# Kernel tuning notes

Measured on AMD Instinct MI355X. Metric: run time of the kernel, lower is better.

The kernel has to match this reference:

```python
import jax, jax.numpy as jnp
import numpy as np


def setup_inputs() -> dict:
    key = jax.random.key(0)
    k1, k2 = jax.random.split(key)
    B, D = 8192, 256
    pred = jax.random.normal(k1, (B, D), dtype=jnp.float32)
    gt = jax.random.normal(k2, (B, D), dtype=jnp.float32)
    sigma = jnp.ones((), dtype=jnp.float32)  # learned scalar param (dim=1, mode='auto')
    return {"pred": pred, "gt": gt, "sigma": sigma}


def reference(pred, gt, sigma):
    # p, g: [B, D] (flatten from start_dim=1 is identity for 2D inputs)
    p = pred.reshape(pred.shape[0], -1)
    g = gt.reshape(gt.shape[0], -1)
    B, D = p.shape
    noise_var = sigma ** 2
    # MVN(mean=p_i, cov=noise_var*I).log_prob(g_j) in closed form:
    # -0.5 * ||g_j - p_i||^2 / noise_var - 0.5 * D * log(2*pi*noise_var)
    sq_dist = (
        jnp.sum(p * p, axis=-1)[:, None]
        + jnp.sum(g * g, axis=-1)[None, :]
        - 2.0 * (p @ g.T)
    )  # [B, B]
    log_norm = 0.5 * D * jnp.log(2.0 * jnp.pi * noise_var)
    logits = -0.5 * sq_dist / noise_var - log_norm  # [B, B], class dim = 1
    # cross_entropy(logits, arange(B)) = mean_i(-log_softmax(logits)[i, i])
    logp = jax.nn.log_softmax(logits, axis=1)
    loss = -jnp.mean(jnp.diagonal(logp))
    loss = loss * jax.lax.stop_gradient(2.0 * noise_var)
    return loss
```

## Files before the change

### kernel.cpp

```cpp
#include <hip/hip_runtime.h>
#include <hip/hip_fp8.h>


typedef float f32x4 __attribute__((ext_vector_type(4)));
typedef float f32x16 __attribute__((ext_vector_type(16)));
typedef long llong2 __attribute__((ext_vector_type(2)));

#define LN2F 0.6931471805599453f
#define LOG2EF 1.4426950408889634f
#define NB 8192
#define ND 256
#define NCHUNK 32

#define AS1 __attribute__((address_space(1)))
#define AS3 __attribute__((address_space(3)))

__device__ __forceinline__ float fexp2(float x) {
#if __has_builtin(__builtin_amdgcn_exp2f)
  return __builtin_amdgcn_exp2f(x);
#else
  float r;
  asm("v_exp_f32 %0, %1\n\ts_nop 1" : "=v"(r) : "v"(x));
  return r;
#endif
}

__device__ __forceinline__ int pack4_fp8(float a, float b, float c, float d) {
#if __has_builtin(__builtin_amdgcn_cvt_pk_fp8_f32)
  int w = __builtin_amdgcn_cvt_pk_fp8_f32(a, b, 0, false);
  w = __builtin_amdgcn_cvt_pk_fp8_f32(c, d, w, true);
  return w;
#else
  unsigned b0 = __hip_fp8_e4m3(a).__x, b1 = __hip_fp8_e4m3(b).__x;
  unsigned b2 = __hip_fp8_e4m3(c).__x, b3 = __hip_fp8_e4m3(d).__x;
  return (int)(b0 | (b1 << 8) | (b2 << 16) | (b3 << 24));
#endif
}

__global__ __launch_bounds__(256) void vmse_prep(
    const float* __restrict__ pred, const float* __restrict__ gt,
    const float* __restrict__ sigma,
    unsigned char* __restrict__ Ah, unsigned char* __restrict__ Bh,
    float* __restrict__ diag, float* __restrict__ gnorm,
    float* __restrict__ ghs)
{
  const float nv = sigma[0] * sigma[0];
  const float s = LOG2EF / nv;
  const int row = blockIdx.x * 4 + (threadIdx.x >> 6);
  const int l = threadIdx.x & 63;
  const float4 p = *(const float4*)(pred + row * ND + l * 4);
  const float4 g = *(const float4*)(gt   + row * ND + l * 4);
  const int pw = pack4_fp8(p.x * s, p.y * s, p.z * s, p.w * s);
  const int gw = pack4_fp8(g.x, g.y, g.z, g.w);
  const int pos = (l >> 3) * 32 + ((l >> 1) & 1) * 16 + ((l >> 2) & 1) * 8 + (l & 1) * 4;
  *(int*)(Ah + row * ND + pos) = pw;
  *(int*)(Bh + row * ND + pos) = gw;
  float dd = p.x * g.x + p.y * g.y + p.z * g.z + p.w * g.w;
  float gg = g.x * g.x + g.y * g.y + g.z * g.z + g.w * g.w;
  #pragma unroll
  for (int off = 1; off < 64; off <<= 1) {
    dd += __shfl_xor(dd, off);
    gg += __shfl_xor(gg, off);
  }
  if (l == 0) {
    diag[row] = dd;
    gnorm[row] = gg;
    ghs[row] = -0.5f * s * gg;
  }
}

__device__ __forceinline__ void epi16(const f32x16& acc, float& m, float& l) {
  const float mx0 = fmaxf(fmaxf(acc[0], acc[1]), fmaxf(acc[2], acc[3]));
  const float mx1 = fmaxf(fmaxf(acc[4], acc[5]), fmaxf(acc[6], acc[7]));
  const float mx2 = fmaxf(fmaxf(acc[8], acc[9]), fmaxf(acc[10], acc[11]));
  const float mx3 = fmaxf(fmaxf(acc[12], acc[13]), fmaxf(acc[14], acc[15]));
  const float tmax = fmaxf(fmaxf(mx0, mx1), fmaxf(mx2, mx3));
  if (__any(tmax > m + 8.0f)) {
    const float nm = fmaxf(m, tmax);
    l *= fexp2(m - nm);
    m = nm;
  }
  const float e0 = (fexp2(acc[0] - m) + fexp2(acc[1] - m)) +
                   (fexp2(acc[2] - m) + fexp2(acc[3] - m));
  const float e1 = (fexp2(acc[4] - m) + fexp2(acc[5] - m)) +
                   (fexp2(acc[6] - m) + fexp2(acc[7] - m));
  const float e2 = (fexp2(acc[8] - m) + fexp2(acc[9] - m)) +
                   (fexp2(acc[10] - m) + fexp2(acc[11] - m));
  const float e3 = (fexp2(acc[12] - m) + fexp2(acc[13] - m)) +
                   (fexp2(acc[14] - m) + fexp2(acc[15] - m));
  l += (e0 + e1) + (e2 + e3);
}

__global__ __launch_bounds__(512, 4) void vmse_main(
    const unsigned char* __restrict__ Ah, const unsigned char* __restrict__ Bh,
    const float* __restrict__ ghs, float* __restrict__ partial)
{
  __shared__ unsigned char lds[8][32 * 256];
  __shared__ float lds_ghs[256];
  const int tid = threadIdx.x;
  const int lane = tid & 63;
  const int wid = tid >> 6;
  const int rb = blockIdx.x & 31;
  const int ch = blockIdx.x >> 5;
  const int r31 = lane & 31;
  const int hi = lane >> 5;
  const int j0 = ch * 256;

  {
    const int r = wid * 4 + (lane >> 4);
    const int cg = (lane & 15) ^ (r & 7);
    const unsigned char* src = Bh + (size_t)(j0 + r) * ND + cg * 16;
    #pragma unroll
    for (int t = 0; t < 8; ++t)
      __builtin_amdgcn_global_load_lds(
          (const AS1 unsigned int*)(src + t * 8192),
          (AS3 unsigned int*)&lds[t][wid * 1024], 16, 0, 0);
  }
  if (tid < 256) lds_ghs[tid] = ghs[j0 + tid];

  long pf[16];
  {
    const unsigned char* prow = Ah + (size_t)((rb * 256) + (wid * 32) + r31) * ND;
    #pragma unroll
    for (int t2 = 0; t2 < 8; ++t2) {
      const llong2 v = *(const llong2*)(prow + t2 * 32 + hi * 16);
      pf[2 * t2] = v[0];
      pf[2 * t2 + 1] = v[1];
    }
  }

  const int r0b = r31 & 1;
  const int q2 = (r31 >> 1) & 3;
  const char* base = (const char*)&lds[0][0] + r31 * 256 + (hi ^ r0b) * 16;
  const char* pq[4];
  #pragma unroll
  for (int b = 0; b < 4; ++b) pq[b] = base + ((b ^ q2) * 32);

  float m2 = -3.0e38f, l2 = 0.0f;

  __syncthreads();

  const char* gbase = (const char*)lds_ghs + hi * 16;

  #define TILE(ACC, tile)                                                    \
    {                                                                        \
      _Pragma("unroll")                                                      \
      for (int q = 0; q < 4; ++q) {                                          \
        const f32x4 gv = *(const f32x4*)(gbase + (tile) * 128 + q * 32);     \
        ACC[4 * q + 0] = gv[0];                                              \
        ACC[4 * q + 1] = gv[1];                                              \
        ACC[4 * q + 2] = gv[2];                                              \
        ACC[4 * q + 3] = gv[3];                                              \
      }                                                                      \
      _Pragma("unroll")                                                      \
      for (int a = 0; a < 2; ++a) {                                          \
        _Pragma("unroll")                                                    \
        for (int b = 0; b < 4; ++b) {                                        \
          const llong2 g = *(const llong2*)(pq[b] + a * 128 + (tile) * 8192);\
          const int t = 2 * (a * 4 + b);                                     \
          ACC = __builtin_amdgcn_mfma_f32_32x32x16_fp8_fp8(g[0], pf[t], ACC, 0, 0, 0);     \
          ACC = __builtin_amdgcn_mfma_f32_32x32x16_fp8_fp8(g[1], pf[t + 1], ACC, 0, 0, 0); \
        }                                                                    \
      }                                                                      \
    }

  f32x16 accA, accB;
  TILE(accA, 0);
  #pragma unroll
  for (int i = 0; i < 4; ++i) {
    TILE(accB, 2 * i + 1);
    epi16(accA, m2, l2);
    if (2 * i + 2 < 8) {
      TILE(accA, 2 * i + 2);
    }
    epi16(accB, m2, l2);
  }

  {
    const float om = __shfl_xor(m2, 32);
    const float ol = __shfl_xor(l2, 32);
    const float nm = fmaxf(m2, om);
    l2 = l2 * fexp2(m2 - nm) + ol * fexp2(om - nm);
    m2 = nm;
    if (hi == 0) {
      const int row = rb * 256 + wid * 32 + r31;
      partial[row * NCHUNK + ch] = m2 + log2f(l2);
    }
  }
}

__global__ __launch_bounds__(256) void vmse_combine(
    const float* __restrict__ partial, const float* __restrict__ diag,
    const float* __restrict__ gnorm, const float* __restrict__ sigma,
    float* __restrict__ bsum)
{
  const int r = blockIdx.x * 256 + threadIdx.x;
  const float nv = sigma[0] * sigma[0];
  float p[NCHUNK];
  float M = -3.0e38f;
  #pragma unroll
  for (int c = 0; c < NCHUNK; ++c) { p[c] = partial[r * NCHUNK + c]; M = fmaxf(M, p[c]); }
  float ssum = 0.f;
  #pragma unroll
  for (int c = 0; c < NCHUNK; ++c) ssum += exp2f(p[c] - M);
  const float lse2 = M + log2f(ssum);
  const float zii = (diag[r] - 0.5f * gnorm[r]) / nv;
  float contrib = LN2F * lse2 - zii;
  #pragma unroll
  for (int off = 1; off < 64; off <<= 1) contrib += __shfl_xor(contrib, off);
  __shared__ float wsum[4];
  if ((threadIdx.x & 63) == 0) wsum[threadIdx.x >> 6] = contrib;
  __syncthreads();
  if (threadIdx.x == 0)
    bsum[blockIdx.x] = (wsum[0] + wsum[1]) + (wsum[2] + wsum[3]);
}

__global__ __launch_bounds__(64) void vmse_final(
    const float* __restrict__ bsum, const float* __restrict__ sigma,
    float* __restrict__ out)
{
  const int lane = threadIdx.x;
  float v = (lane < 32) ? bsum[lane] : 0.f;
  #pragma unroll
  for (int off = 1; off < 64; off <<= 1) v += __shfl_xor(v, off);
  if (lane == 0) {
    const float nv = sigma[0] * sigma[0];
    out[0] = v * (2.0f * nv / (float)NB);
  }
}

extern "C" void kernel_launch(void* const* d_in, const int* in_sizes, int n_in,
                              void* d_out, int out_size, void* d_ws, size_t ws_size,
                              hipStream_t stream)
{
  const float* pred  = (const float*)d_in[0];
  const float* gt    = (const float*)d_in[1];
  const float* sigma = (const float*)d_in[2];
  char* ws = (char*)d_ws;
  unsigned char* Ah = (unsigned char*)(ws);
  unsigned char* Bh = (unsigned char*)(ws + (2u << 20));
  float* gnorm   = (float*)(ws + (4u << 20));
  float* diag    = (float*)(ws + (4u << 20) + (32u << 10));
  float* ghs     = (float*)(ws + (4u << 20) + (64u << 10));
  float* partial = (float*)(ws + (4u << 20) + (96u << 10));
  float* bsum    = (float*)(ws + (4u << 20) + (96u << 10) + (1u << 20));

  vmse_prep<<<NB / 4, 256, 0, stream>>>(pred, gt, sigma, Ah, Bh, diag, gnorm, ghs);
  vmse_main<<<32 * NCHUNK, 512, 0, stream>>>(Ah, Bh, ghs, partial);
  vmse_combine<<<NB / 256, 256, 0, stream>>>(partial, diag, gnorm, sigma, bsum);
  vmse_final<<<1, 64, 0, stream>>>(bsum, sigma, (float*)d_out);
}
```

Measured before the change: 43.74 us.

## Use gfx950 scaled 32x32x64 FP8 MFMA with matching operand layout and swizzle

Replaces the 32x32x16 FP8 MFMA sequence with the MI355X scaled 32x32x64 f8f6f4 MFMA, using unit scales (0x7F exponent), so each tile needs 4 instead of 16 MFMA issues. The prep kernel now writes FP8 data in natural row order, and the LDS swizzle and per-lane load addressing are reworked to feed 32-byte operands per lane. The aim is higher matrix throughput and fewer instructions. The risk is a wrong layout mapping or extra LDS bank conflicts from the new swizzle.

```diff
diff --git a/kernel.cpp b/kernel.cpp
--- a/kernel.cpp
+++ b/kernel.cpp
@@ -4,7 +4,8 @@
 
 typedef float f32x4 __attribute__((ext_vector_type(4)));
 typedef float f32x16 __attribute__((ext_vector_type(16)));
-typedef long llong2 __attribute__((ext_vector_type(2)));
+typedef int i32x4 __attribute__((ext_vector_type(4)));
+typedef int i32x8 __attribute__((ext_vector_type(8)));
 
 #define LN2F 0.6931471805599453f
 #define LOG2EF 1.4426950408889634f
@@ -52,9 +53,8 @@
   const float4 g = *(const float4*)(gt   + row * ND + l * 4);
   const int pw = pack4_fp8(p.x * s, p.y * s, p.z * s, p.w * s);
   const int gw = pack4_fp8(g.x, g.y, g.z, g.w);
-  const int pos = (l >> 3) * 32 + ((l >> 1) & 1) * 16 + ((l >> 2) & 1) * 8 + (l & 1) * 4;
-  *(int*)(Ah + row * ND + pos) = pw;
-  *(int*)(Bh + row * ND + pos) = gw;
+  *(int*)(Ah + row * ND + l * 4) = pw;
+  *(int*)(Bh + row * ND + l * 4) = gw;
   float dd = p.x * g.x + p.y * g.y + p.z * g.z + p.w * g.w;
   float gg = g.x * g.x + g.y * g.y + g.z * g.z + g.w * g.w;
   #pragma unroll
@@ -108,7 +108,7 @@
 
   {
     const int r = wid * 4 + (lane >> 4);
-    const int cg = (lane & 15) ^ (r & 7);
+    const int cg = (lane & 15) ^ (r & 15);
     const unsigned char* src = Bh + (size_t)(j0 + r) * ND + cg * 16;
     #pragma unroll
     for (int t = 0; t < 8; ++t)
@@ -118,23 +118,26 @@
   }
   if (tid < 256) lds_ghs[tid] = ghs[j0 + tid];
 
-  long pf[16];
+  i32x8 pf[4];
   {
     const unsigned char* prow = Ah + (size_t)((rb * 256) + (wid * 32) + r31) * ND;
     #pragma unroll
-    for (int t2 = 0; t2 < 8; ++t2) {
-      const llong2 v = *(const llong2*)(prow + t2 * 32 + hi * 16);
-      pf[2 * t2] = v[0];
-      pf[2 * t2 + 1] = v[1];
-    }
-  }
-
-  const int r0b = r31 & 1;
-  const int q2 = (r31 >> 1) & 3;
-  const char* base = (const char*)&lds[0][0] + r31 * 256 + (hi ^ r0b) * 16;
-  const char* pq[4];
-  #pragma unroll
-  for (int b = 0; b < 4; ++b) pq[b] = base + ((b ^ q2) * 32);
+    for (int m = 0; m < 4; ++m)
+      pf[m] = *(const i32x8*)(prow + m * 64 + hi * 32);
+  }
+
+  const int sl = r31 & 3;
+  const int sh = (r31 >> 2) & 3;
+  const char* ldsc = (const char*)&lds[0][0];
+  const char* pj0 = ldsc + r31 * 256 + (((hi * 2) ^ sl) * 16);
+  const char* pj1 = ldsc + r31 * 256 + (((hi * 2 + 1) ^ sl) * 16);
+  const char* pg0[4];
+  const char* pg1[4];
+  #pragma unroll
+  for (int m = 0; m < 4; ++m) {
+    pg0[m] = pj0 + ((m ^ sh) << 6);
+    pg1[m] = pj1 + ((m ^ sh) << 6);
+  }
 
   float m2 = -3.0e38f, l2 = 0.0f;
 
@@ -153,14 +156,13 @@
         ACC[4 * q + 3] = gv[3];                                              \
       }                                                                      \
       _Pragma("unroll")                                                      \
-      for (int a = 0; a < 2; ++a) {                                          \
-        _Pragma("unroll")                                                    \
-        for (int b = 0; b < 4; ++b) {                                        \
-          const llong2 g = *(const llong2*)(pq[b] + a * 128 + (tile) * 8192);\
-          const int t = 2 * (a * 4 + b);                                     \
-          ACC = __builtin_amdgcn_mfma_f32_32x32x16_fp8_fp8(g[0], pf[t], ACC, 0, 0, 0);     \
-          ACC = __builtin_amdgcn_mfma_f32_32x32x16_fp8_fp8(g[1], pf[t + 1], ACC, 0, 0, 0); \
-        }                                                                    \
+      for (int m = 0; m < 4; ++m) {                                          \
+        const i32x4 a0 = *(const i32x4*)(pg0[m] + (tile) * 8192);            \
+        const i32x4 a1 = *(const i32x4*)(pg1[m] + (tile) * 8192);            \
+        const i32x8 ga = {a0[0], a0[1], a0[2], a0[3],                        \
+                          a1[0], a1[1], a1[2], a1[3]};                       \
+        ACC = __builtin_amdgcn_mfma_scale_f32_32x32x64_f8f6f4(               \
+            ga, pf[m], ACC, 0, 0, 0, 0x7F7F7F7F, 0, 0x7F7F7F7F);             \
       }                                                                      \
     }
 
```

Result: faster. 38.47 us (median of 2 runs) (-12.1%).
